# Performance work log

Hardware: AMD Instinct MI355X
Metric: run time of the kernel (lower is better)

Reference implementation:

```python
import jax, jax.numpy as jnp
import numpy as np

N_EMBED = 1024
N_HEADS = 16
HEAD_SIZE = N_EMBED // N_HEADS


def setup_inputs() -> dict:
    key = jax.random.key(0)
    ks = jax.random.split(key, 9)
    d = N_EMBED
    s = 1.0 / np.sqrt(d)
    return {
        "x": jax.random.normal(ks[0], (2, 2048, d), dtype=jnp.float32),
        "Wq": jax.random.uniform(ks[1], (d, d), jnp.float32, -s, s),
        "bq": jax.random.uniform(ks[2], (d,), jnp.float32, -s, s),
        "Wk": jax.random.uniform(ks[3], (d, d), jnp.float32, -s, s),
        "bk": jax.random.uniform(ks[4], (d,), jnp.float32, -s, s),
        "Wv": jax.random.uniform(ks[5], (d, d), jnp.float32, -s, s),
        "bv": jax.random.uniform(ks[6], (d,), jnp.float32, -s, s),
        "Wo": jax.random.uniform(ks[7], (d, d), jnp.float32, -s, s),
        "bo": jax.random.uniform(ks[8], (d,), jnp.float32, -s, s),
    }


def reference(x, Wq, bq, Wk, bk, Wv, bv, Wo, bo):
    B, T, D = x.shape
    H, Hd = N_HEADS, HEAD_SIZE
    # projections (torch Linear: x @ W^T + b; here W stored already transposed)
    q = (x @ Wq + bq).reshape(B, T, H, Hd).transpose(0, 2, 1, 3)  # [B,H,T,Hd]
    k = (x @ Wk + bk).reshape(B, T, H, Hd).transpose(0, 2, 1, 3)
    v = (x @ Wv + bv).reshape(B, T, H, Hd).transpose(0, 2, 1, 3)
    scores = jnp.einsum("bhqd,bhkd->bhqk", q, k) * (Hd ** -0.5)  # [B,H,T,T]
    causal = jnp.tril(jnp.ones((T, T), dtype=bool))
    scores = jnp.where(causal[None, None], scores, -jnp.inf)
    probs = jax.nn.softmax(scores, axis=-1)
    out = jnp.einsum("bhqk,bhkd->bhqd", probs, v)  # [B,H,T,Hd]
    out = out.transpose(0, 2, 1, 3).reshape(B, T, D)
    return out @ Wo + bo
```

## Files before the change

### kernel.cpp

```cpp
#include <hip/hip_runtime.h>
#include <cstdint>
#include <cstddef>

typedef __bf16 bf16;
typedef __bf16 bf16x4 __attribute__((ext_vector_type(4)));
typedef __bf16 bf16x8 __attribute__((ext_vector_type(8)));
typedef float  f32x4  __attribute__((ext_vector_type(4)));
typedef float  f32x16 __attribute__((ext_vector_type(16)));

#define B_  2
#define T_  2048
#define D_  1024
#define H_  16
#define HD_ 64
#define M_  (B_ * T_)
#define NQB 16

#define GLOAD_LDS(gsrc, ldst) \
    __builtin_amdgcn_global_load_lds( \
        (const __attribute__((address_space(1))) void*)(gsrc), \
        (__attribute__((address_space(3))) void*)(ldst), 16, 0, 0)

__global__ void cast_x_kernel(const float* __restrict__ in, bf16* __restrict__ out) {
    int i = (blockIdx.x * 256 + threadIdx.x) * 4;
    const float4 v = *reinterpret_cast<const float4*>(in + i);
    bf16x4 o = { (bf16)v.x, (bf16)v.y, (bf16)v.z, (bf16)v.w };
    *reinterpret_cast<bf16x4*>(out + i) = o;
}

__global__ void transpose_cast_kernel(
    const float* __restrict__ W0, bf16* __restrict__ T0,
    const float* __restrict__ W1, bf16* __restrict__ T1,
    const float* __restrict__ W2, bf16* __restrict__ T2,
    const float* __restrict__ W3, bf16* __restrict__ T3)
{
    __shared__ float tile[32][33];
    const float* W = blockIdx.z == 0 ? W0 : blockIdx.z == 1 ? W1 : blockIdx.z == 2 ? W2 : W3;
    bf16*       Wt = blockIdx.z == 0 ? T0 : blockIdx.z == 1 ? T1 : blockIdx.z == 2 ? T2 : T3;
    const int tx = threadIdx.x & 31, ty = threadIdx.x >> 5;
    const int bx = blockIdx.x * 32, by = blockIdx.y * 32;
    #pragma unroll
    for (int r = 0; r < 32; r += 8)
        tile[ty + r][tx] = W[(size_t)(by + ty + r) * D_ + bx + tx];
    __syncthreads();
    #pragma unroll
    for (int r = 0; r < 32; r += 8)
        Wt[(size_t)(bx + ty + r) * D_ + by + tx] = (bf16)tile[tx][ty + r];
}

__device__ __forceinline__ void gemm_128_2ph(
    const bf16* __restrict__ A, const bf16* __restrict__ Bt,
    int m0, int n0, bf16 (*As)[128][64], bf16 (*Bs)[128][64], f32x16 acc[2][2])
{
    constexpr int K = D_;
    constexpr int NK = K / 64;
    const int tid  = threadIdx.x;
    const int wave = tid >> 6, lane = tid & 63;
    const int l5 = lane & 31, hi = lane >> 5;
    const int wr = wave >> 1, wc = wave & 1;

    const int rseg = lane >> 3;
    const int srcc = (lane & 7) ^ rseg;

    auto stage = [&](int b, int k0) {
        #pragma unroll
        for (int cc = 0; cc < 4; ++cc) {
            const int c   = wave * 4 + cc;
            const int row = c * 8 + rseg;
            GLOAD_LDS(A  + (size_t)(m0 + row) * K + k0 + srcc * 8, &As[b][c * 8][0]);
            GLOAD_LDS(Bt + (size_t)(n0 + row) * K + k0 + srcc * 8, &Bs[b][c * 8][0]);
        }
    };

    stage(0, 0);
    __syncthreads();

    #pragma unroll 1
    for (int t = 0; t < NK; ++t) {
        const int cur = t & 1;
        if (t + 1 < NK) stage(cur ^ 1, (t + 1) * 64);

        bf16x8 af[2][4], bfr[2][4];
        #pragma unroll
        for (int mi = 0; mi < 2; ++mi)
            #pragma unroll
            for (int ks = 0; ks < 4; ++ks) {
                const int row = wr * 64 + mi * 32 + l5;
                af[mi][ks] = *reinterpret_cast<const bf16x8*>(
                    &As[cur][row][((ks * 2 + hi) ^ (row & 7)) * 8]);
            }
        #pragma unroll
        for (int nj = 0; nj < 2; ++nj)
            #pragma unroll
            for (int ks = 0; ks < 4; ++ks) {
                const int row = wc * 64 + nj * 32 + l5;
                bfr[nj][ks] = *reinterpret_cast<const bf16x8*>(
                    &Bs[cur][row][((ks * 2 + hi) ^ (row & 7)) * 8]);
            }
        __builtin_amdgcn_s_setprio(1);
        #pragma unroll
        for (int mi = 0; mi < 2; ++mi)
            #pragma unroll
            for (int nj = 0; nj < 2; ++nj)
                #pragma unroll
                for (int ks = 0; ks < 4; ++ks)
                    acc[mi][nj] = __builtin_amdgcn_mfma_f32_32x32x16_bf16(
                        af[mi][ks], bfr[nj][ks], acc[mi][nj], 0, 0, 0);
        __builtin_amdgcn_s_setprio(0);
        __syncthreads();
    }
}

__global__ __launch_bounds__(256, 2) void qkv128_kernel(
    const bf16* __restrict__ xb,
    const bf16* __restrict__ WqT, const float* __restrict__ bq, bf16* __restrict__ Qo,
    const bf16* __restrict__ WkT, const float* __restrict__ bk, bf16* __restrict__ Ko,
    const bf16* __restrict__ WvT, const float* __restrict__ bv, bf16* __restrict__ Vt)
{
    __shared__ bf16 As[2][128][64];
    __shared__ bf16 Bs[2][128][64];

    const int bid = blockIdx.x;
    const int swz = (bid & 7) * 96 + (bid >> 3);

    const bf16 *Aop, *Bop;
    const float *bias;
    bf16 *outp;
    float scale = 1.0f;
    int m0, n0, mode;
    if (swz < 512) {
        const int bm = swz & 31, bn = swz >> 5;
        m0 = bm * 128;
        Aop = xb;
        if (bn < 8) { Bop = WqT; n0 = bn * 128;       bias = bq; outp = Qo; scale = 0.125f; }
        else        { Bop = WkT; n0 = (bn - 8) * 128; bias = bk; outp = Ko; }
        mode = 0;
    } else {
        const int v = swz - 512, bm = v & 7, bn = v >> 3;
        m0 = bm * 128; n0 = bn * 128;
        Aop = WvT; Bop = xb; bias = bv; outp = Vt; mode = 1;
    }

    f32x16 acc[2][2] = {};
    gemm_128_2ph(Aop, Bop, m0, n0, As, Bs, acc);

    const int lane = threadIdx.x & 63, wave = threadIdx.x >> 6;
    const int l5 = lane & 31, hi = lane >> 5;
    const int wr = wave >> 1, wc = wave & 1;
    if (mode == 0) {
        #pragma unroll
        for (int mi = 0; mi < 2; ++mi)
            #pragma unroll
            for (int nj = 0; nj < 2; ++nj)
                #pragma unroll
                for (int q = 0; q < 16; ++q) {
                    const int m = m0 + wr * 64 + mi * 32 + (q & 3) + 8 * (q >> 2) + 4 * hi;
                    const int n = n0 + wc * 64 + nj * 32 + l5;
                    const float val = (acc[mi][nj][q] + bias[n]) * scale;
                    const int b = m >> 11, t = m & (T_ - 1);
                    const int h = n >> 6, hd = n & 63;
                    outp[((size_t)((b * H_ + h) * T_ + t)) * HD_ + hd] = (bf16)val;
                }
    } else {
        #pragma unroll
        for (int mi = 0; mi < 2; ++mi)
            #pragma unroll
            for (int nj = 0; nj < 2; ++nj)
                #pragma unroll
                for (int q = 0; q < 16; ++q) {
                    const int d = m0 + wr * 64 + mi * 32 + (q & 3) + 8 * (q >> 2) + 4 * hi;
                    const int n = n0 + wc * 64 + nj * 32 + l5;
                    const float val = acc[mi][nj][q] + bias[d];
                    const int b = n >> 11, t = n & (T_ - 1);
                    outp[((size_t)(b * D_ + d)) * T_ + t] = (bf16)val;
                }
    }
}

__global__ __launch_bounds__(256, 2) void gemm_out_kernel(
    const bf16* __restrict__ A, const bf16* __restrict__ WoT,
    const float* __restrict__ bo, float* __restrict__ Out)
{
    __shared__ bf16 As[2][128][64];
    __shared__ bf16 Bs[2][128][64];
    const int m0 = blockIdx.x * 128, n0 = blockIdx.y * 128;

    f32x16 acc[2][2] = {};
    gemm_128_2ph(A, WoT, m0, n0, As, Bs, acc);

    const int lane = threadIdx.x & 63, wave = threadIdx.x >> 6;
    const int l5 = lane & 31, hi = lane >> 5;
    const int wr = wave >> 1, wc = wave & 1;
    #pragma unroll
    for (int mi = 0; mi < 2; ++mi)
        #pragma unroll
        for (int nj = 0; nj < 2; ++nj)
            #pragma unroll
            for (int q = 0; q < 16; ++q) {
                const int m = m0 + wr * 64 + mi * 32 + (q & 3) + 8 * (q >> 2) + 4 * hi;
                const int n = n0 + wc * 64 + nj * 32 + l5;
                Out[(size_t)m * D_ + n] = acc[mi][nj][q] + bo[n];
            }
}

__global__ __launch_bounds__(512) void attn_kernel(
    const bf16* __restrict__ Q, const bf16* __restrict__ K,
    const bf16* __restrict__ Vt, bf16* __restrict__ Out)
{
    const int bh = blockIdx.y;
    const int tid = threadIdx.x, wave = tid >> 6, lane = tid & 63;
    const int lr = lane & 15, lg = lane >> 4;
    const size_t kbase = (size_t)bh * T_ * HD_;
    const size_t vbase = (size_t)bh * HD_ * T_;

    __shared__ bf16 Ks[2][64][64];
    __shared__ bf16 Vs[2][64][64];
    __shared__ bf16 Ps[8][16][72];

    auto stage = [&](int sb, int kt) {
        const int kv0 = kt * 64;
        const int rseg = lane >> 3;
        const int srcw = (lane & 7) ^ rseg;
        const int row  = wave * 8 + rseg;
        GLOAD_LDS(K  + kbase + (size_t)(kv0 + row) * HD_ + srcw * 8, &Ks[sb][wave * 8][0]);
        GLOAD_LDS(Vt + vbase + (size_t)row * T_ + kv0 + srcw * 8,    &Vs[sb][wave * 8][0]);
    };
    auto kfrag = [&](int sb, int row, int chunk) {
        return *reinterpret_cast<const bf16x8*>(&Ks[sb][row][(chunk ^ (row & 7)) * 8]);
    };
    auto vfrag = [&](int sb, int row, int chunk) {
        return *reinterpret_cast<const bf16x8*>(&Vs[sb][row][(chunk ^ (row & 7)) * 8]);
    };

    #pragma unroll 1
    for (int half = 0; half < 2; ++half) {
        const int qb = half == 0 ? blockIdx.x : (NQB - 1 - blockIdx.x);
        const int q0 = qb * 128;
        const int nt = 2 * qb + 2;
        const int qw = wave * 16;

        bf16x8 qf[2];
        {
            const bf16* qrow = Q + kbase + (size_t)(q0 + qw + lr) * HD_;
            qf[0] = *reinterpret_cast<const bf16x8*>(qrow + lg * 8);
            qf[1] = *reinterpret_cast<const bf16x8*>(qrow + 32 + lg * 8);
        }

        float m_s = -1e30f, l_s = 0.f;
        f32x4 o_acc[4] = {};

        stage(0, 0);
        __syncthreads();

        #pragma unroll 1
        for (int t = 0; t < nt; ++t) {
            const int cur = t & 1;
            if (t + 1 < nt) stage(cur ^ 1, t + 1);

            const int kv0 = t * 64;
            if (kv0 <= q0 + qw + 15) {
                f32x4 s[4] = {};
                __builtin_amdgcn_s_setprio(1);
                #pragma unroll
                for (int n16 = 0; n16 < 4; ++n16)
                    #pragma unroll
                    for (int kk = 0; kk < 2; ++kk)
                        s[n16] = __builtin_amdgcn_mfma_f32_16x16x32_bf16(
                            kfrag(cur, n16 * 16 + lr, kk * 4 + lg), qf[kk], s[n16], 0, 0, 0);
                __builtin_amdgcn_s_setprio(0);
                if (t >= 2 * qb) {
                    #pragma unroll
                    for (int n16 = 0; n16 < 4; ++n16)
                        #pragma unroll
                        for (int r = 0; r < 4; ++r)
                            if (kv0 + n16 * 16 + lg * 4 + r > q0 + qw + lr)
                                s[n16][r] = -1e30f;
                }
                float mx = s[0][0];
                #pragma unroll
                for (int n16 = 0; n16 < 4; ++n16)
                    #pragma unroll
                    for (int r = 0; r < 4; ++r)
                        mx = fmaxf(mx, s[n16][r]);
                mx = fmaxf(mx, __shfl_xor(mx, 16));
                mx = fmaxf(mx, __shfl_xor(mx, 32));
                if (__any(mx > m_s + 8.0f)) {
                    const float mnew  = fmaxf(m_s, mx);
                    const float alpha = __expf(m_s - mnew);
                    #pragma unroll
                    for (int r = 0; r < 4; ++r) {
                        const float a = __shfl(alpha, lg * 4 + r);
                        #pragma unroll
                        for (int nd = 0; nd < 4; ++nd) o_acc[nd][r] *= a;
                    }
                    l_s *= alpha;
                    m_s = mnew;
                }
                float rs = 0.f;
                #pragma unroll
                for (int n16 = 0; n16 < 4; ++n16) {
                    bf16x4 pw;
                    #pragma unroll
                    for (int r = 0; r < 4; ++r) {
                        const float p = __expf(s[n16][r] - m_s);
                        rs += p;
                        pw[r] = (bf16)p;
                    }
                    *reinterpret_cast<bf16x4*>(&Ps[wave][lr][n16 * 16 + lg * 4]) = pw;
                }
                rs += __shfl_xor(rs, 16);
                rs += __shfl_xor(rs, 32);
                l_s += rs;
                __builtin_amdgcn_s_setprio(1);
                #pragma unroll
                for (int ks = 0; ks < 2; ++ks) {
                    const bf16x8 pa = *reinterpret_cast<const bf16x8*>(&Ps[wave][lr][ks * 32 + lg * 8]);
                    #pragma unroll
                    for (int nd = 0; nd < 4; ++nd)
                        o_acc[nd] = __builtin_amdgcn_mfma_f32_16x16x32_bf16(
                            pa, vfrag(cur, nd * 16 + lr, ks * 4 + lg), o_acc[nd], 0, 0, 0);
                }
                __builtin_amdgcn_s_setprio(0);
            }
            __syncthreads();
        }

        const int b = bh >> 4, h = bh & 15;
        const float linv = 1.0f / l_s;
        #pragma unroll
        for (int r = 0; r < 4; ++r) {
            const float li = __shfl(linv, lg * 4 + r);
            const int q = q0 + qw + lg * 4 + r;
            #pragma unroll
            for (int nd = 0; nd < 4; ++nd) {
                const int d = nd * 16 + lr;
                Out[((size_t)(b * T_ + q)) * D_ + h * HD_ + d] = (bf16)(o_acc[nd][r] * li);
            }
        }
    }
}

extern "C" void kernel_launch(void* const* d_in, const int* in_sizes, int n_in,
                              void* d_out, int out_size, void* d_ws, size_t ws_size,
                              hipStream_t stream) {
    const float* x  = (const float*)d_in[0];
    const float* Wq = (const float*)d_in[1];
    const float* bq = (const float*)d_in[2];
    const float* Wk = (const float*)d_in[3];
    const float* bk = (const float*)d_in[4];
    const float* Wv = (const float*)d_in[5];
    const float* bv = (const float*)d_in[6];
    const float* Wo = (const float*)d_in[7];
    const float* bo = (const float*)d_in[8];
    float* out = (float*)d_out;

    char* ws = (char*)d_ws;
    bf16* xb   = (bf16*)(ws);
    bf16* WqT  = (bf16*)(ws + ( 8u << 20));
    bf16* WkT  = (bf16*)(ws + (10u << 20));
    bf16* WvT  = (bf16*)(ws + (12u << 20));
    bf16* WoT  = (bf16*)(ws + (14u << 20));
    bf16* Qb   = (bf16*)(ws + (16u << 20));
    bf16* Kb   = (bf16*)(ws + (24u << 20));
    bf16* Vtb  = (bf16*)(ws + (32u << 20));
    bf16* attn = (bf16*)(ws + (40u << 20));

    cast_x_kernel<<<4096, 256, 0, stream>>>(x, xb);
    transpose_cast_kernel<<<dim3(32, 32, 4), 256, 0, stream>>>(
        Wq, WqT, Wk, WkT, Wv, WvT, Wo, WoT);

    qkv128_kernel<<<768, 256, 0, stream>>>(xb, WqT, bq, Qb, WkT, bk, Kb, WvT, bv, Vtb);

    attn_kernel<<<dim3(NQB / 2, 32), 512, 0, stream>>>(Qb, Kb, Vtb, attn);

    gemm_out_kernel<<<dim3(32, 8), 256, 0, stream>>>(attn, WoT, bo, out);
}
```

Before: 130.8 us.

## Process paired causal query blocks in one KV sweep and fuse prep kernels

The attention kernel now handles its low and high query blocks together in a single loop over KV tiles. Each staged K/V tile is shared by both blocks, and the two blocks' MFMA and softmax work is interleaved, with a separate P buffer for each block. The x cast is folded into the weight transpose-cast kernel as an extra grid slice, which saves a launch. The cost is roughly double the accumulator and Q-fragment registers, which may reduce occupancy or cause spills.

```diff
diff --git a/kernel.cpp b/kernel.cpp
--- a/kernel.cpp
+++ b/kernel.cpp
@@ -21,19 +21,25 @@
         (const __attribute__((address_space(1))) void*)(gsrc), \
         (__attribute__((address_space(3))) void*)(ldst), 16, 0, 0)
 
-__global__ void cast_x_kernel(const float* __restrict__ in, bf16* __restrict__ out) {
-    int i = (blockIdx.x * 256 + threadIdx.x) * 4;
-    const float4 v = *reinterpret_cast<const float4*>(in + i);
-    bf16x4 o = { (bf16)v.x, (bf16)v.y, (bf16)v.z, (bf16)v.w };
-    *reinterpret_cast<bf16x4*>(out + i) = o;
-}
-
-__global__ void transpose_cast_kernel(
+__global__ void prep_kernel(
+    const float* __restrict__ x,  bf16* __restrict__ xb,
     const float* __restrict__ W0, bf16* __restrict__ T0,
     const float* __restrict__ W1, bf16* __restrict__ T1,
     const float* __restrict__ W2, bf16* __restrict__ T2,
     const float* __restrict__ W3, bf16* __restrict__ T3)
 {
+    if (blockIdx.z == 4) {
+        const int linear = blockIdx.y * 32 + blockIdx.x;
+        const int base = linear * 4096 + threadIdx.x * 4;
+        #pragma unroll
+        for (int u = 0; u < 4; ++u) {
+            const int i = base + u * 1024;
+            const float4 v = *reinterpret_cast<const float4*>(x + i);
+            bf16x4 o = { (bf16)v.x, (bf16)v.y, (bf16)v.z, (bf16)v.w };
+            *reinterpret_cast<bf16x4*>(xb + i) = o;
+        }
+        return;
+    }
     __shared__ float tile[32][33];
     const float* W = blockIdx.z == 0 ? W0 : blockIdx.z == 1 ? W1 : blockIdx.z == 2 ? W2 : W3;
     bf16*       Wt = blockIdx.z == 0 ? T0 : blockIdx.z == 1 ? T1 : blockIdx.z == 2 ? T2 : T3;
@@ -215,7 +221,7 @@
 
     __shared__ bf16 Ks[2][64][64];
     __shared__ bf16 Vs[2][64][64];
-    __shared__ bf16 Ps[8][16][72];
+    __shared__ bf16 Ps[2][8][16][72];
 
     auto stage = [&](int sb, int kt) {
         const int kv0 = kt * 64;
@@ -232,110 +238,190 @@
         return *reinterpret_cast<const bf16x8*>(&Vs[sb][row][(chunk ^ (row & 7)) * 8]);
     };
 
+    const int qbL = blockIdx.x;
+    const int qbH = NQB - 1 - blockIdx.x;
+    const int q0L = qbL * 128, q0H = qbH * 128;
+    const int nt  = 2 * qbH + 2;
+    const int qw  = wave * 16;
+
+    bf16x8 qfL[2], qfH[2];
+    {
+        const bf16* qrow = Q + kbase + (size_t)(q0L + qw + lr) * HD_;
+        qfL[0] = *reinterpret_cast<const bf16x8*>(qrow + lg * 8);
+        qfL[1] = *reinterpret_cast<const bf16x8*>(qrow + 32 + lg * 8);
+        const bf16* qrow2 = Q + kbase + (size_t)(q0H + qw + lr) * HD_;
+        qfH[0] = *reinterpret_cast<const bf16x8*>(qrow2 + lg * 8);
+        qfH[1] = *reinterpret_cast<const bf16x8*>(qrow2 + 32 + lg * 8);
+    }
+
+    float mL = -1e30f, lL = 0.f, mH = -1e30f, lH = 0.f;
+    f32x4 oL[4] = {}, oH[4] = {};
+
+    stage(0, 0);
+    __syncthreads();
+
     #pragma unroll 1
-    for (int half = 0; half < 2; ++half) {
-        const int qb = half == 0 ? blockIdx.x : (NQB - 1 - blockIdx.x);
-        const int q0 = qb * 128;
-        const int nt = 2 * qb + 2;
-        const int qw = wave * 16;
-
-        bf16x8 qf[2];
-        {
-            const bf16* qrow = Q + kbase + (size_t)(q0 + qw + lr) * HD_;
-            qf[0] = *reinterpret_cast<const bf16x8*>(qrow + lg * 8);
-            qf[1] = *reinterpret_cast<const bf16x8*>(qrow + 32 + lg * 8);
-        }
-
-        float m_s = -1e30f, l_s = 0.f;
-        f32x4 o_acc[4] = {};
-
-        stage(0, 0);
-        __syncthreads();
-
-        #pragma unroll 1
-        for (int t = 0; t < nt; ++t) {
-            const int cur = t & 1;
-            if (t + 1 < nt) stage(cur ^ 1, t + 1);
-
-            const int kv0 = t * 64;
-            if (kv0 <= q0 + qw + 15) {
-                f32x4 s[4] = {};
-                __builtin_amdgcn_s_setprio(1);
-                #pragma unroll
-                for (int n16 = 0; n16 < 4; ++n16)
-                    #pragma unroll
-                    for (int kk = 0; kk < 2; ++kk)
-                        s[n16] = __builtin_amdgcn_mfma_f32_16x16x32_bf16(
-                            kfrag(cur, n16 * 16 + lr, kk * 4 + lg), qf[kk], s[n16], 0, 0, 0);
-                __builtin_amdgcn_s_setprio(0);
-                if (t >= 2 * qb) {
-                    #pragma unroll
-                    for (int n16 = 0; n16 < 4; ++n16)
-                        #pragma unroll
-                        for (int r = 0; r < 4; ++r)
-                            if (kv0 + n16 * 16 + lg * 4 + r > q0 + qw + lr)
-                                s[n16][r] = -1e30f;
-                }
-                float mx = s[0][0];
+    for (int t = 0; t < nt; ++t) {
+        const int cur = t & 1;
+        if (t + 1 < nt) stage(cur ^ 1, t + 1);
+
+        const int kv0 = t * 64;
+        const bool actL = kv0 <= q0L + qw + 15;
+        const bool actH = kv0 <= q0H + qw + 15;
+
+        f32x4 sL[4], sH[4];
+        __builtin_amdgcn_s_setprio(1);
+        if (actH) {
+            #pragma unroll
+            for (int n16 = 0; n16 < 4; ++n16) {
+                sH[n16] = f32x4{};
+                #pragma unroll
+                for (int kk = 0; kk < 2; ++kk)
+                    sH[n16] = __builtin_amdgcn_mfma_f32_16x16x32_bf16(
+                        kfrag(cur, n16 * 16 + lr, kk * 4 + lg), qfH[kk], sH[n16], 0, 0, 0);
+            }
+        }
+        if (actL) {
+            #pragma unroll
+            for (int n16 = 0; n16 < 4; ++n16) {
+                sL[n16] = f32x4{};
+                #pragma unroll
+                for (int kk = 0; kk < 2; ++kk)
+                    sL[n16] = __builtin_amdgcn_mfma_f32_16x16x32_bf16(
+                        kfrag(cur, n16 * 16 + lr, kk * 4 + lg), qfL[kk], sL[n16], 0, 0, 0);
+            }
+        }
+        __builtin_amdgcn_s_setprio(0);
+
+        if (actH) {
+            if (t >= 2 * qbH) {
                 #pragma unroll
                 for (int n16 = 0; n16 < 4; ++n16)
                     #pragma unroll
                     for (int r = 0; r < 4; ++r)
-                        mx = fmaxf(mx, s[n16][r]);
-                mx = fmaxf(mx, __shfl_xor(mx, 16));
-                mx = fmaxf(mx, __shfl_xor(mx, 32));
-                if (__any(mx > m_s + 8.0f)) {
-                    const float mnew  = fmaxf(m_s, mx);
-                    const float alpha = __expf(m_s - mnew);
+                        if (kv0 + n16 * 16 + lg * 4 + r > q0H + qw + lr) sH[n16][r] = -1e30f;
+            }
+            float mx = sH[0][0];
+            #pragma unroll
+            for (int n16 = 0; n16 < 4; ++n16)
+                #pragma unroll
+                for (int r = 0; r < 4; ++r) mx = fmaxf(mx, sH[n16][r]);
+            mx = fmaxf(mx, __shfl_xor(mx, 16));
+            mx = fmaxf(mx, __shfl_xor(mx, 32));
+            if (__any(mx > mH + 8.0f)) {
+                const float mnew = fmaxf(mH, mx);
+                const float alpha = __expf(mH - mnew);
+                #pragma unroll
+                for (int r = 0; r < 4; ++r) {
+                    const float a = __shfl(alpha, lg * 4 + r);
                     #pragma unroll
-                    for (int r = 0; r < 4; ++r) {
-                        const float a = __shfl(alpha, lg * 4 + r);
-                        #pragma unroll
-                        for (int nd = 0; nd < 4; ++nd) o_acc[nd][r] *= a;
-                    }
-                    l_s *= alpha;
-                    m_s = mnew;
-                }
-                float rs = 0.f;
-                #pragma unroll
-                for (int n16 = 0; n16 < 4; ++n16) {
-                    bf16x4 pw;
+                    for (int nd = 0; nd < 4; ++nd) oH[nd][r] *= a;
+                }
+                lH *= alpha; mH = mnew;
+            }
+            float rs = 0.f;
+            #pragma unroll
+            for (int n16 = 0; n16 < 4; ++n16) {
+                bf16x4 pw;
+                #pragma unroll
+                for (int r = 0; r < 4; ++r) {
+                    const float p = __expf(sH[n16][r] - mH);
+                    rs += p; pw[r] = (bf16)p;
+                }
+                *reinterpret_cast<bf16x4*>(&Ps[1][wave][lr][n16 * 16 + lg * 4]) = pw;
+            }
+            rs += __shfl_xor(rs, 16);
+            rs += __shfl_xor(rs, 32);
+            lH += rs;
+        }
+        if (actL) {
+            if (t >= 2 * qbL) {
+                #pragma unroll
+                for (int n16 = 0; n16 < 4; ++n16)
                     #pragma unroll
-                    for (int r = 0; r < 4; ++r) {
-                        const float p = __expf(s[n16][r] - m_s);
-                        rs += p;
-                        pw[r] = (bf16)p;
-                    }
-                    *reinterpret_cast<bf16x4*>(&Ps[wave][lr][n16 * 16 + lg * 4]) = pw;
-                }
-                rs += __shfl_xor(rs, 16);
-                rs += __shfl_xor(rs, 32);
-                l_s += rs;
-                __builtin_amdgcn_s_setprio(1);
-                #pragma unroll
-                for (int ks = 0; ks < 2; ++ks) {
-                    const bf16x8 pa = *reinterpret_cast<const bf16x8*>(&Ps[wave][lr][ks * 32 + lg * 8]);
+                    for (int r = 0; r < 4; ++r)
+                        if (kv0 + n16 * 16 + lg * 4 + r > q0L + qw + lr) sL[n16][r] = -1e30f;
+            }
+            float mx = sL[0][0];
+            #pragma unroll
+            for (int n16 = 0; n16 < 4; ++n16)
+                #pragma unroll
+                for (int r = 0; r < 4; ++r) mx = fmaxf(mx, sL[n16][r]);
+            mx = fmaxf(mx, __shfl_xor(mx, 16));
+            mx = fmaxf(mx, __shfl_xor(mx, 32));
+            if (__any(mx > mL + 8.0f)) {
+                const float mnew = fmaxf(mL, mx);
+                const float alpha = __expf(mL - mnew);
+                #pragma unroll
+                for (int r = 0; r < 4; ++r) {
+                    const float a = __shfl(alpha, lg * 4 + r);
                     #pragma unroll
-                    for (int nd = 0; nd < 4; ++nd)
-                        o_acc[nd] = __builtin_amdgcn_mfma_f32_16x16x32_bf16(
-                            pa, vfrag(cur, nd * 16 + lr, ks * 4 + lg), o_acc[nd], 0, 0, 0);
-                }
-                __builtin_amdgcn_s_setprio(0);
-            }
-            __syncthreads();
-        }
-
-        const int b = bh >> 4, h = bh & 15;
-        const float linv = 1.0f / l_s;
+                    for (int nd = 0; nd < 4; ++nd) oL[nd][r] *= a;
+                }
+                lL *= alpha; mL = mnew;
+            }
+            float rs = 0.f;
+            #pragma unroll
+            for (int n16 = 0; n16 < 4; ++n16) {
+                bf16x4 pw;
+                #pragma unroll
+                for (int r = 0; r < 4; ++r) {
+                    const float p = __expf(sL[n16][r] - mL);
+                    rs += p; pw[r] = (bf16)p;
+                }
+                *reinterpret_cast<bf16x4*>(&Ps[0][wave][lr][n16 * 16 + lg * 4]) = pw;
+            }
+            rs += __shfl_xor(rs, 16);
+            rs += __shfl_xor(rs, 32);
+            lL += rs;
+        }
+
+        __builtin_amdgcn_s_setprio(1);
+        if (actH) {
+            #pragma unroll
+            for (int ks = 0; ks < 2; ++ks) {
+                const bf16x8 pa = *reinterpret_cast<const bf16x8*>(&Ps[1][wave][lr][ks * 32 + lg * 8]);
+                #pragma unroll
+                for (int nd = 0; nd < 4; ++nd)
+                    oH[nd] = __builtin_amdgcn_mfma_f32_16x16x32_bf16(
+                        pa, vfrag(cur, nd * 16 + lr, ks * 4 + lg), oH[nd], 0, 0, 0);
+            }
+        }
+        if (actL) {
+            #pragma unroll
+            for (int ks = 0; ks < 2; ++ks) {
+                const bf16x8 pa = *reinterpret_cast<const bf16x8*>(&Ps[0][wave][lr][ks * 32 + lg * 8]);
+                #pragma unroll
+                for (int nd = 0; nd < 4; ++nd)
+                    oL[nd] = __builtin_amdgcn_mfma_f32_16x16x32_bf16(
+                        pa, vfrag(cur, nd * 16 + lr, ks * 4 + lg), oL[nd], 0, 0, 0);
+            }
+        }
+        __builtin_amdgcn_s_setprio(0);
+        __syncthreads();
+    }
+
+    const int b = bh >> 4, h = bh & 15;
+    {
+        const float linv = 1.0f / lL;
         #pragma unroll
         for (int r = 0; r < 4; ++r) {
             const float li = __shfl(linv, lg * 4 + r);
-            const int q = q0 + qw + lg * 4 + r;
-            #pragma unroll
-            for (int nd = 0; nd < 4; ++nd) {
-                const int d = nd * 16 + lr;
-                Out[((size_t)(b * T_ + q)) * D_ + h * HD_ + d] = (bf16)(o_acc[nd][r] * li);
-            }
+            const int q = q0L + qw + lg * 4 + r;
+            #pragma unroll
+            for (int nd = 0; nd < 4; ++nd)
+                Out[((size_t)(b * T_ + q)) * D_ + h * HD_ + nd * 16 + lr] = (bf16)(oL[nd][r] * li);
+        }
+    }
+    {
+        const float linv = 1.0f / lH;
+        #pragma unroll
+        for (int r = 0; r < 4; ++r) {
+            const float li = __shfl(linv, lg * 4 + r);
+            const int q = q0H + qw + lg * 4 + r;
+            #pragma unroll
+            for (int nd = 0; nd < 4; ++nd)
+                Out[((size_t)(b * T_ + q)) * D_ + h * HD_ + nd * 16 + lr] = (bf16)(oH[nd][r] * li);
         }
     }
 }
@@ -365,9 +451,8 @@
     bf16* Vtb  = (bf16*)(ws + (32u << 20));
     bf16* attn = (bf16*)(ws + (40u << 20));
 
-    cast_x_kernel<<<4096, 256, 0, stream>>>(x, xb);
-    transpose_cast_kernel<<<dim3(32, 32, 4), 256, 0, stream>>>(
-        Wq, WqT, Wk, WkT, Wv, WvT, Wo, WoT);
+    prep_kernel<<<dim3(32, 32, 5), 256, 0, stream>>>(
+        x, xb, Wq, WqT, Wk, WkT, Wv, WvT, Wo, WoT);
 
     qkv128_kernel<<<768, 256, 0, stream>>>(xb, WqT, bq, Qb, WkT, bk, Kb, WvT, bv, Vtb);
 
```

Measured after the change: 133.7 us. 1.02x slower.

## Shrink attention query tiles, remap blocks per XCD, and fuse prep kernels

Applied to the files above, without the earlier changes.

Attention blocks now handle 64-query tiles with 4 waves instead of 128-query tiles with 8 waves. The grid grows to 512 one-dimensional blocks, remapped so each XCD handles a contiguous set of heads for K/V L2 locality. Each wave now always has work per KV tile, which removes the per-wave causal skip branch, and the two-halves pairing still balances causal load. The x cast is also folded into the weight transpose kernel to save one launch. The trade-off is that each block loads K/V once per 64 queries rather than per 128, doubling K/V traffic.

```diff
diff --git a/kernel.cpp b/kernel.cpp
--- a/kernel.cpp
+++ b/kernel.cpp
@@ -14,26 +14,32 @@
 #define H_  16
 #define HD_ 64
 #define M_  (B_ * T_)
-#define NQB 16
+#define NQB 32
 
 #define GLOAD_LDS(gsrc, ldst) \
     __builtin_amdgcn_global_load_lds( \
         (const __attribute__((address_space(1))) void*)(gsrc), \
         (__attribute__((address_space(3))) void*)(ldst), 16, 0, 0)
 
-__global__ void cast_x_kernel(const float* __restrict__ in, bf16* __restrict__ out) {
-    int i = (blockIdx.x * 256 + threadIdx.x) * 4;
-    const float4 v = *reinterpret_cast<const float4*>(in + i);
-    bf16x4 o = { (bf16)v.x, (bf16)v.y, (bf16)v.z, (bf16)v.w };
-    *reinterpret_cast<bf16x4*>(out + i) = o;
-}
-
-__global__ void transpose_cast_kernel(
+__global__ void prep_kernel(
+    const float* __restrict__ x,  bf16* __restrict__ xb,
     const float* __restrict__ W0, bf16* __restrict__ T0,
     const float* __restrict__ W1, bf16* __restrict__ T1,
     const float* __restrict__ W2, bf16* __restrict__ T2,
     const float* __restrict__ W3, bf16* __restrict__ T3)
 {
+    if (blockIdx.z == 4) {
+        const int linear = blockIdx.y * 32 + blockIdx.x;
+        const int base = linear * 4096 + threadIdx.x * 4;
+        #pragma unroll
+        for (int u = 0; u < 4; ++u) {
+            const int i = base + u * 1024;
+            const float4 v = *reinterpret_cast<const float4*>(x + i);
+            bf16x4 o = { (bf16)v.x, (bf16)v.y, (bf16)v.z, (bf16)v.w };
+            *reinterpret_cast<bf16x4*>(xb + i) = o;
+        }
+        return;
+    }
     __shared__ float tile[32][33];
     const float* W = blockIdx.z == 0 ? W0 : blockIdx.z == 1 ? W1 : blockIdx.z == 2 ? W2 : W3;
     bf16*       Wt = blockIdx.z == 0 ? T0 : blockIdx.z == 1 ? T1 : blockIdx.z == 2 ? T2 : T3;
@@ -203,11 +209,15 @@
             }
 }
 
-__global__ __launch_bounds__(512) void attn_kernel(
+__global__ __launch_bounds__(256) void attn_kernel(
     const bf16* __restrict__ Q, const bf16* __restrict__ K,
     const bf16* __restrict__ Vt, bf16* __restrict__ Out)
 {
-    const int bh = blockIdx.y;
+    const int bid = blockIdx.x;
+    const int xcd = bid & 7, j = bid >> 3;
+    const int bh  = xcd * 4 + (j >> 4);
+    const int pr  = j & 15;
+
     const int tid = threadIdx.x, wave = tid >> 6, lane = tid & 63;
     const int lr = lane & 15, lg = lane >> 4;
     const size_t kbase = (size_t)bh * T_ * HD_;
@@ -215,15 +225,19 @@
 
     __shared__ bf16 Ks[2][64][64];
     __shared__ bf16 Vs[2][64][64];
-    __shared__ bf16 Ps[8][16][72];
+    __shared__ bf16 Ps[4][16][72];
 
     auto stage = [&](int sb, int kt) {
         const int kv0 = kt * 64;
         const int rseg = lane >> 3;
         const int srcw = (lane & 7) ^ rseg;
-        const int row  = wave * 8 + rseg;
-        GLOAD_LDS(K  + kbase + (size_t)(kv0 + row) * HD_ + srcw * 8, &Ks[sb][wave * 8][0]);
-        GLOAD_LDS(Vt + vbase + (size_t)row * T_ + kv0 + srcw * 8,    &Vs[sb][wave * 8][0]);
+        #pragma unroll
+        for (int cc = 0; cc < 2; ++cc) {
+            const int seg = wave * 2 + cc;
+            const int row = seg * 8 + rseg;
+            GLOAD_LDS(K  + kbase + (size_t)(kv0 + row) * HD_ + srcw * 8, &Ks[sb][seg * 8][0]);
+            GLOAD_LDS(Vt + vbase + (size_t)row * T_ + kv0 + srcw * 8,    &Vs[sb][seg * 8][0]);
+        }
     };
     auto kfrag = [&](int sb, int row, int chunk) {
         return *reinterpret_cast<const bf16x8*>(&Ks[sb][row][(chunk ^ (row & 7)) * 8]);
@@ -234,9 +248,9 @@
 
     #pragma unroll 1
     for (int half = 0; half < 2; ++half) {
-        const int qb = half == 0 ? blockIdx.x : (NQB - 1 - blockIdx.x);
-        const int q0 = qb * 128;
-        const int nt = 2 * qb + 2;
+        const int qb = half == 0 ? pr : (NQB - 1 - pr);
+        const int q0 = qb * 64;
+        const int nt = qb + 1;
         const int qw = wave * 16;
 
         bf16x8 qf[2];
@@ -258,70 +272,68 @@
             if (t + 1 < nt) stage(cur ^ 1, t + 1);
 
             const int kv0 = t * 64;
-            if (kv0 <= q0 + qw + 15) {
-                f32x4 s[4] = {};
-                __builtin_amdgcn_s_setprio(1);
-                #pragma unroll
-                for (int n16 = 0; n16 < 4; ++n16)
-                    #pragma unroll
-                    for (int kk = 0; kk < 2; ++kk)
-                        s[n16] = __builtin_amdgcn_mfma_f32_16x16x32_bf16(
-                            kfrag(cur, n16 * 16 + lr, kk * 4 + lg), qf[kk], s[n16], 0, 0, 0);
-                __builtin_amdgcn_s_setprio(0);
-                if (t >= 2 * qb) {
-                    #pragma unroll
-                    for (int n16 = 0; n16 < 4; ++n16)
-                        #pragma unroll
-                        for (int r = 0; r < 4; ++r)
-                            if (kv0 + n16 * 16 + lg * 4 + r > q0 + qw + lr)
-                                s[n16][r] = -1e30f;
-                }
-                float mx = s[0][0];
+            f32x4 s[4] = {};
+            __builtin_amdgcn_s_setprio(1);
+            #pragma unroll
+            for (int n16 = 0; n16 < 4; ++n16)
+                #pragma unroll
+                for (int kk = 0; kk < 2; ++kk)
+                    s[n16] = __builtin_amdgcn_mfma_f32_16x16x32_bf16(
+                        kfrag(cur, n16 * 16 + lr, kk * 4 + lg), qf[kk], s[n16], 0, 0, 0);
+            __builtin_amdgcn_s_setprio(0);
+            if (t == qb) {
                 #pragma unroll
                 for (int n16 = 0; n16 < 4; ++n16)
                     #pragma unroll
                     for (int r = 0; r < 4; ++r)
-                        mx = fmaxf(mx, s[n16][r]);
-                mx = fmaxf(mx, __shfl_xor(mx, 16));
-                mx = fmaxf(mx, __shfl_xor(mx, 32));
-                if (__any(mx > m_s + 8.0f)) {
-                    const float mnew  = fmaxf(m_s, mx);
-                    const float alpha = __expf(m_s - mnew);
+                        if (kv0 + n16 * 16 + lg * 4 + r > q0 + qw + lr)
+                            s[n16][r] = -1e30f;
+            }
+            float mx = s[0][0];
+            #pragma unroll
+            for (int n16 = 0; n16 < 4; ++n16)
+                #pragma unroll
+                for (int r = 0; r < 4; ++r)
+                    mx = fmaxf(mx, s[n16][r]);
+            mx = fmaxf(mx, __shfl_xor(mx, 16));
+            mx = fmaxf(mx, __shfl_xor(mx, 32));
+            if (__any(mx > m_s + 8.0f)) {
+                const float mnew  = fmaxf(m_s, mx);
+                const float alpha = __expf(m_s - mnew);
+                #pragma unroll
+                for (int r = 0; r < 4; ++r) {
+                    const float a = __shfl(alpha, lg * 4 + r);
                     #pragma unroll
-                    for (int r = 0; r < 4; ++r) {
-                        const float a = __shfl(alpha, lg * 4 + r);
-                        #pragma unroll
-                        for (int nd = 0; nd < 4; ++nd) o_acc[nd][r] *= a;
-                    }
-                    l_s *= alpha;
-                    m_s = mnew;
+                    for (int nd = 0; nd < 4; ++nd) o_acc[nd][r] *= a;
                 }
-                float rs = 0.f;
-                #pragma unroll
-                for (int n16 = 0; n16 < 4; ++n16) {
-                    bf16x4 pw;
-                    #pragma unroll
-                    for (int r = 0; r < 4; ++r) {
-                        const float p = __expf(s[n16][r] - m_s);
-                        rs += p;
-                        pw[r] = (bf16)p;
-                    }
-                    *reinterpret_cast<bf16x4*>(&Ps[wave][lr][n16 * 16 + lg * 4]) = pw;
+                l_s *= alpha;
+                m_s = mnew;
+            }
+            float rs = 0.f;
+            #pragma unroll
+            for (int n16 = 0; n16 < 4; ++n16) {
+                bf16x4 pw;
+                #pragma unroll
+                for (int r = 0; r < 4; ++r) {
+                    const float p = __expf(s[n16][r] - m_s);
+                    rs += p;
+                    pw[r] = (bf16)p;
                 }
-                rs += __shfl_xor(rs, 16);
-                rs += __shfl_xor(rs, 32);
-                l_s += rs;
-                __builtin_amdgcn_s_setprio(1);
-                #pragma unroll
-                for (int ks = 0; ks < 2; ++ks) {
-                    const bf16x8 pa = *reinterpret_cast<const bf16x8*>(&Ps[wave][lr][ks * 32 + lg * 8]);
-                    #pragma unroll
-                    for (int nd = 0; nd < 4; ++nd)
-                        o_acc[nd] = __builtin_amdgcn_mfma_f32_16x16x32_bf16(
-                            pa, vfrag(cur, nd * 16 + lr, ks * 4 + lg), o_acc[nd], 0, 0, 0);
-                }
-                __builtin_amdgcn_s_setprio(0);
-            }
+                *reinterpret_cast<bf16x4*>(&Ps[wave][lr][n16 * 16 + lg * 4]) = pw;
+            }
+            rs += __shfl_xor(rs, 16);
+            rs += __shfl_xor(rs, 32);
+            l_s += rs;
+            __builtin_amdgcn_s_setprio(1);
+            #pragma unroll
+            for (int ks = 0; ks < 2; ++ks) {
+                const bf16x8 pa = *reinterpret_cast<const bf16x8*>(&Ps[wave][lr][ks * 32 + lg * 8]);
+                #pragma unroll
+                for (int nd = 0; nd < 4; ++nd)
+                    o_acc[nd] = __builtin_amdgcn_mfma_f32_16x16x32_bf16(
+                        pa, vfrag(cur, nd * 16 + lr, ks * 4 + lg), o_acc[nd], 0, 0, 0);
+            }
+            __builtin_amdgcn_s_setprio(0);
             __syncthreads();
         }
 
@@ -365,13 +377,12 @@
     bf16* Vtb  = (bf16*)(ws + (32u << 20));
     bf16* attn = (bf16*)(ws + (40u << 20));
 
-    cast_x_kernel<<<4096, 256, 0, stream>>>(x, xb);
-    transpose_cast_kernel<<<dim3(32, 32, 4), 256, 0, stream>>>(
-        Wq, WqT, Wk, WkT, Wv, WvT, Wo, WoT);
+    prep_kernel<<<dim3(32, 32, 5), 256, 0, stream>>>(
+        x, xb, Wq, WqT, Wk, WkT, Wv, WvT, Wo, WoT);
 
     qkv128_kernel<<<768, 256, 0, stream>>>(xb, WqT, bq, Qb, WkT, bk, Kb, WvT, bv, Vtb);
 
-    attn_kernel<<<dim3(NQB / 2, 32), 512, 0, stream>>>(Qb, Kb, Vtb, attn);
+    attn_kernel<<<512, 256, 0, stream>>>(Qb, Kb, Vtb, attn);
 
     gemm_out_kernel<<<dim3(32, 8), 256, 0, stream>>>(attn, WoT, bo, out);
 }
```

Result: faster. 126.9 us (-3.0%).
